# Kernel optimization log

Hardware: AMD Instinct MI355X
Metric: run time of the kernel (lower is better)

The kernel has to match this reference:

```python
import jax, jax.numpy as jnp
import numpy as np


def _build_cayley(metric):
    """Cayley table for the Clifford algebra with diagonal metric.
    Blades are indexed by bitmask (0=scalar, 1=e1, 2=e2, 3=e12, 4=e3, ...).
    cayley[i, j, k] = coefficient of blade j in the geometric product e_i * e_k.
    """
    n = len(metric)
    dim = 1 << n
    c = np.zeros((dim, dim, dim), dtype=np.float32)
    for a in range(dim):
        for b in range(dim):
            sign = 1.0
            tmp = a >> 1
            while tmp:  # count basis-vector swaps needed to sort e_a e_b
                if bin(tmp & b).count('1') & 1:
                    sign = -sign
                tmp >>= 1
            common = a & b
            for i in range(n):  # contract repeated basis vectors via the metric
                if common & (1 << i):
                    sign *= metric[i]
            c[a, a ^ b, b] = sign
    return c


def fast_einsum(q_einsum, cayley, k_einsum):
    # geometric product of two multivectors (same einsum as the torch.jit version)
    return jnp.einsum('...i,ijk,...k->...j', q_einsum, cayley, k_einsum)


def _embed_grade1(x, mv_dim):
    # embed a 3D vector as a grade-1 multivector: components at blade bitmasks 1, 2, 4
    mv = jnp.zeros(x.shape[:-1] + (mv_dim,), x.dtype)
    mv = mv.at[..., 1].set(x[..., 0])
    mv = mv.at[..., 2].set(x[..., 1])
    mv = mv.at[..., 4].set(x[..., 2])
    return mv


def setup_inputs() -> dict:
    key = jax.random.key(0)
    k1, k2 = jax.random.split(key)
    B, P, D = 4, 8192, 3
    return {
        'source_cloud': jax.random.normal(k1, (B, P, D), dtype=jnp.float32),
        'target_cloud': jax.random.normal(k2, (B, P, D), dtype=jnp.float32),
        'cayley': jnp.asarray(_build_cayley([1.0, 1.0, 1.0])),  # (8,8,8)
    }


def reference(source_cloud, target_cloud, cayley):
    # KNN (K=1) via full pairwise squared distances: (B, P1, P2)
    d2 = (jnp.sum(source_cloud * source_cloud, -1)[:, :, None]
          + jnp.sum(target_cloud * target_cloud, -1)[:, None, :]
          - 2.0 * jnp.einsum('bid,bjd->bij', source_cloud, target_cloud))
    idx = jnp.argmin(d2, axis=2)  # (B, P1) nearest-neighbor indices (non-differentiable)
    # knn_gather: nn[b, i] = target_cloud[b, idx[b, i]]
    nn = jnp.take_along_axis(target_cloud, idx[..., None], axis=1)  # (B, P1, 3)
    # multivector residual and geometric product with itself via the Cayley table
    diff_mv = _embed_grade1(source_cloud - nn, cayley.shape[0])  # (B, P1, 8)
    gp = fast_einsum(diff_mv, cayley, diff_mv)  # (B, P1, 8)
    # scalar part of v*v equals ||v||^2 under the Euclidean metric
    per_point = gp[..., 0]
    per_cloud = jnp.sum(per_point, axis=1)  # point_reduction='sum'
    return jnp.mean(per_cloud)  # batch_reduction='mean'
```

## Files before the change

### kernel.cpp

```cpp
#include <hip/hip_runtime.h>

#define BATCH 4
#define NPTS 8192
#define NTOT (BATCH * NPTS)

constexpr int THREADS   = 256;
constexpr int S_PER_THR = 8;
constexpr int SRC_CHUNK = THREADS * S_PER_THR;
constexpr int NSC       = NPTS / SRC_CHUNK;
constexpr int TGT_CHUNK = 256;
constexpr int NTC       = NPTS / TGT_CHUNK;
constexpr int R1_BLOCKS = 64;

__global__ __launch_bounds__(THREADS) void knn_partial_kernel(
        const float* __restrict__ src,
        const float* __restrict__ tgt,
        float* __restrict__ ws)
{
    int bid = blockIdx.x;
    int tc  = bid % NTC;
    int sc  = (bid / NTC) % NSC;
    int b   = bid / (NTC * NSC);

    __shared__ float4 tsh[TGT_CHUNK];

    {
        const float* tbase = tgt + ((size_t)b * NPTS + (size_t)tc * TGT_CHUNK) * 3;
        int k = threadIdx.x;
        float x = tbase[3 * k + 0];
        float y = tbase[3 * k + 1];
        float z = tbase[3 * k + 2];
        tsh[k] = make_float4(x, y, z, 0.5f * (x * x + y * y + z * z));
    }

    const float* sbase = src + ((size_t)b * NPTS + (size_t)sc * SRC_CHUNK) * 3;
    float sx[S_PER_THR], sy[S_PER_THR], sz[S_PER_THR], mb[S_PER_THR];
    #pragma unroll
    for (int s = 0; s < S_PER_THR; ++s) {
        int i = threadIdx.x + s * THREADS;
        sx[s] = sbase[3 * i + 0];
        sy[s] = sbase[3 * i + 1];
        sz[s] = sbase[3 * i + 2];
        mb[s] = INFINITY;
    }
    __syncthreads();

    #pragma unroll 4
    for (int j = 0; j < TGT_CHUNK; j += 2) {
        float4 t0 = tsh[j];
        float4 t1 = tsh[j + 1];
        #pragma unroll
        for (int s = 0; s < S_PER_THR; ++s) {
            float m0 = fmaf(-sx[s], t0.x, fmaf(-sy[s], t0.y, fmaf(-sz[s], t0.z, t0.w)));
            float m1 = fmaf(-sx[s], t1.x, fmaf(-sy[s], t1.y, fmaf(-sz[s], t1.z, t1.w)));
            mb[s] = fminf(mb[s], fminf(m0, m1));
        }
    }

    float* wbase = ws + (size_t)tc * NTOT + (size_t)b * NPTS + (size_t)sc * SRC_CHUNK;
    #pragma unroll
    for (int s = 0; s < S_PER_THR; ++s) {
        float hs = 0.5f * (sx[s] * sx[s] + sy[s] * sy[s] + sz[s] * sz[s]);
        wbase[threadIdx.x + s * THREADS] = mb[s] + hs;
    }
}

__global__ __launch_bounds__(256) void reduce1_kernel(
        const float* __restrict__ ws,
        float* __restrict__ partials)
{
    __shared__ float acc[256];
    int base = blockIdx.x * (NTOT / R1_BLOCKS);
    float a = 0.0f;
    #pragma unroll
    for (int p = 0; p < 2; ++p) {
        int i = base + threadIdx.x + p * 256;
        float m = INFINITY;
        #pragma unroll
        for (int sl = 0; sl < NTC; ++sl)
            m = fminf(m, ws[(size_t)sl * NTOT + i]);
        a += m;
    }
    acc[threadIdx.x] = a;
    __syncthreads();
    for (int off = 128; off > 0; off >>= 1) {
        if (threadIdx.x < off) acc[threadIdx.x] += acc[threadIdx.x + off];
        __syncthreads();
    }
    if (threadIdx.x == 0) partials[blockIdx.x] = acc[0];
}

__global__ __launch_bounds__(64) void reduce2_kernel(
        const float* __restrict__ partials,
        float* __restrict__ out)
{
    float v = partials[threadIdx.x];
    #pragma unroll
    for (int off = 32; off > 0; off >>= 1)
        v += __shfl_down(v, off, 64);
    if (threadIdx.x == 0) out[0] = v * 0.5f;
}

extern "C" void kernel_launch(void* const* d_in, const int* in_sizes, int n_in,
                              void* d_out, int out_size, void* d_ws, size_t ws_size,
                              hipStream_t stream) {
    const float* src = (const float*)d_in[0];
    const float* tgt = (const float*)d_in[1];
    float* out = (float*)d_out;
    float* ws  = (float*)d_ws;
    float* partials = (float*)((char*)d_ws + (size_t)NTC * NTOT * sizeof(float));

    knn_partial_kernel<<<BATCH * NSC * NTC, THREADS, 0, stream>>>(src, tgt, ws);
    reduce1_kernel<<<R1_BLOCKS, 256, 0, stream>>>(ws, partials);
    reduce2_kernel<<<1, 64, 0, stream>>>(partials, out);
}
```

Before: 33.17 us.

## Halve target chunk size and fuse final reductions with last-block atomic counter

Halves the target tile per block, which doubles the KNN grid to 512 blocks and adds occupancy launch bounds. This is meant to fill the GPU's compute units better, at the cost of twice as many partial-min slices to write and reduce. The two reduction kernels are merged into one: the last block to finish, found with an atomic counter and thread fences, does the final sum. That removes a launch but adds a memset to reset the counter. The reduction now uses 128 blocks, each handling one point per thread across 64 slices.

Result: slower. 49.25 us (+48.5%).

```diff
diff --git a/kernel.cpp b/kernel.cpp
--- a/kernel.cpp
+++ b/kernel.cpp
@@ -8,11 +8,11 @@
 constexpr int S_PER_THR = 8;
 constexpr int SRC_CHUNK = THREADS * S_PER_THR;
 constexpr int NSC       = NPTS / SRC_CHUNK;
-constexpr int TGT_CHUNK = 256;
+constexpr int TGT_CHUNK = 128;
 constexpr int NTC       = NPTS / TGT_CHUNK;
-constexpr int R1_BLOCKS = 64;
+constexpr int RBLOCKS   = 128;
 
-__global__ __launch_bounds__(THREADS) void knn_partial_kernel(
+__global__ __launch_bounds__(THREADS, 4) void knn_partial_kernel(
         const float* __restrict__ src,
         const float* __restrict__ tgt,
         float* __restrict__ ws)
@@ -24,7 +24,7 @@
 
     __shared__ float4 tsh[TGT_CHUNK];
 
-    {
+    if (threadIdx.x < TGT_CHUNK) {
         const float* tbase = tgt + ((size_t)b * NPTS + (size_t)tc * TGT_CHUNK) * 3;
         int k = threadIdx.x;
         float x = tbase[3 * k + 0];
@@ -65,40 +65,46 @@
     }
 }
 
-__global__ __launch_bounds__(256) void reduce1_kernel(
+__global__ __launch_bounds__(256) void reduce_kernel(
         const float* __restrict__ ws,
-        float* __restrict__ partials)
+        float* __restrict__ partials,
+        unsigned* __restrict__ counter,
+        float* __restrict__ out)
 {
     __shared__ float acc[256];
-    int base = blockIdx.x * (NTOT / R1_BLOCKS);
-    float a = 0.0f;
-    #pragma unroll
-    for (int p = 0; p < 2; ++p) {
-        int i = base + threadIdx.x + p * 256;
-        float m = INFINITY;
-        #pragma unroll
-        for (int sl = 0; sl < NTC; ++sl)
-            m = fminf(m, ws[(size_t)sl * NTOT + i]);
-        a += m;
-    }
-    acc[threadIdx.x] = a;
+    __shared__ unsigned my_rank;
+
+    int i = blockIdx.x * 256 + threadIdx.x;
+    float m = INFINITY;
+    #pragma unroll 8
+    for (int sl = 0; sl < NTC; ++sl)
+        m = fminf(m, ws[(size_t)sl * NTOT + i]);
+
+    acc[threadIdx.x] = m;
     __syncthreads();
     for (int off = 128; off > 0; off >>= 1) {
         if (threadIdx.x < off) acc[threadIdx.x] += acc[threadIdx.x + off];
         __syncthreads();
     }
-    if (threadIdx.x == 0) partials[blockIdx.x] = acc[0];
-}
+    if (threadIdx.x == 0) {
+        atomicExch(&partials[blockIdx.x], acc[0]);
+        __threadfence();
+        my_rank = atomicAdd(counter, 1u);
+    }
+    __syncthreads();
 
-__global__ __launch_bounds__(64) void reduce2_kernel(
-        const float* __restrict__ partials,
-        float* __restrict__ out)
-{
-    float v = partials[threadIdx.x];
-    #pragma unroll
-    for (int off = 32; off > 0; off >>= 1)
-        v += __shfl_down(v, off, 64);
-    if (threadIdx.x == 0) out[0] = v * 0.5f;
+    if (my_rank == RBLOCKS - 1) {
+        __threadfence();
+        float v = (threadIdx.x < RBLOCKS) ? atomicAdd(&partials[threadIdx.x], 0.0f)
+                                          : 0.0f;
+        acc[threadIdx.x] = v;
+        __syncthreads();
+        for (int off = 128; off > 0; off >>= 1) {
+            if (threadIdx.x < off) acc[threadIdx.x] += acc[threadIdx.x + off];
+            __syncthreads();
+        }
+        if (threadIdx.x == 0) out[0] = acc[0] * 0.5f;
+    }
 }
 
 extern "C" void kernel_launch(void* const* d_in, const int* in_sizes, int n_in,
@@ -107,10 +113,13 @@
     const float* src = (const float*)d_in[0];
     const float* tgt = (const float*)d_in[1];
     float* out = (float*)d_out;
-    float* ws  = (float*)d_ws;
-    float* partials = (float*)((char*)d_ws + (size_t)NTC * NTOT * sizeof(float));
+
+    float*    ws       = (float*)d_ws;
+    float*    partials = (float*)((char*)d_ws + (size_t)NTC * NTOT * 4);
+    unsigned* counter  = (unsigned*)((char*)partials + RBLOCKS * 4);
+
+    hipMemsetAsync(counter, 0, sizeof(unsigned), stream);
 
     knn_partial_kernel<<<BATCH * NSC * NTC, THREADS, 0, stream>>>(src, tgt, ws);
-    reduce1_kernel<<<R1_BLOCKS, 256, 0, stream>>>(ws, partials);
-    reduce2_kernel<<<1, 64, 0, stream>>>(partials, out);
+    reduce_kernel<<<RBLOCKS, 256, 0, stream>>>(ws, partials, counter, out);
 }
```

## Precompute packed target float4s in prep kernel and read them directly from global

Applied to the files above, without the earlier changes.

Adds a prep kernel that packs each target point into a float4 holding the coordinates and half its squared norm. The KNN kernel then drops its LDS staging and __syncthreads and reads those float4s straight from global memory as uniform loads. The target chunk is halved, which doubles the block count, and the reduction is reorganised into 128 blocks with one point per thread. The costs are an extra kernel launch, a larger workspace, twice as many partial-min slices to reduce, and global or scalar-cache loads in the inner loop instead of LDS reads.

Result: slower. 54.95 us (+65.7%).

```diff
diff --git a/kernel.cpp b/kernel.cpp
--- a/kernel.cpp
+++ b/kernel.cpp
@@ -8,30 +8,30 @@
 constexpr int S_PER_THR = 8;
 constexpr int SRC_CHUNK = THREADS * S_PER_THR;
 constexpr int NSC       = NPTS / SRC_CHUNK;
-constexpr int TGT_CHUNK = 256;
+constexpr int TGT_CHUNK = 128;
 constexpr int NTC       = NPTS / TGT_CHUNK;
-constexpr int R1_BLOCKS = 64;
+constexpr int RBLOCKS   = 128;
+
+__global__ __launch_bounds__(256) void prep_kernel(
+        const float* __restrict__ tgt, float4* __restrict__ tq) {
+    int i = blockIdx.x * 256 + threadIdx.x;
+    if (i < NTOT) {
+        float x = tgt[3 * i + 0];
+        float y = tgt[3 * i + 1];
+        float z = tgt[3 * i + 2];
+        tq[i] = make_float4(x, y, z, 0.5f * (x * x + y * y + z * z));
+    }
+}
 
 __global__ __launch_bounds__(THREADS) void knn_partial_kernel(
         const float* __restrict__ src,
-        const float* __restrict__ tgt,
+        const float4* __restrict__ tq,
         float* __restrict__ ws)
 {
     int bid = blockIdx.x;
     int tc  = bid % NTC;
     int sc  = (bid / NTC) % NSC;
     int b   = bid / (NTC * NSC);
-
-    __shared__ float4 tsh[TGT_CHUNK];
-
-    {
-        const float* tbase = tgt + ((size_t)b * NPTS + (size_t)tc * TGT_CHUNK) * 3;
-        int k = threadIdx.x;
-        float x = tbase[3 * k + 0];
-        float y = tbase[3 * k + 1];
-        float z = tbase[3 * k + 2];
-        tsh[k] = make_float4(x, y, z, 0.5f * (x * x + y * y + z * z));
-    }
 
     const float* sbase = src + ((size_t)b * NPTS + (size_t)sc * SRC_CHUNK) * 3;
     float sx[S_PER_THR], sy[S_PER_THR], sz[S_PER_THR], mb[S_PER_THR];
@@ -43,12 +43,13 @@
         sz[s] = sbase[3 * i + 2];
         mb[s] = INFINITY;
     }
-    __syncthreads();
+
+    const float4* tbase = tq + (size_t)b * NPTS + (size_t)tc * TGT_CHUNK;
 
     #pragma unroll 4
     for (int j = 0; j < TGT_CHUNK; j += 2) {
-        float4 t0 = tsh[j];
-        float4 t1 = tsh[j + 1];
+        float4 t0 = tbase[j];
+        float4 t1 = tbase[j + 1];
         #pragma unroll
         for (int s = 0; s < S_PER_THR; ++s) {
             float m0 = fmaf(-sx[s], t0.x, fmaf(-sy[s], t0.y, fmaf(-sz[s], t0.z, t0.w)));
@@ -70,18 +71,12 @@
         float* __restrict__ partials)
 {
     __shared__ float acc[256];
-    int base = blockIdx.x * (NTOT / R1_BLOCKS);
-    float a = 0.0f;
-    #pragma unroll
-    for (int p = 0; p < 2; ++p) {
-        int i = base + threadIdx.x + p * 256;
-        float m = INFINITY;
-        #pragma unroll
-        for (int sl = 0; sl < NTC; ++sl)
-            m = fminf(m, ws[(size_t)sl * NTOT + i]);
-        a += m;
-    }
-    acc[threadIdx.x] = a;
+    int i = blockIdx.x * 256 + threadIdx.x;
+    float m = INFINITY;
+    #pragma unroll 8
+    for (int sl = 0; sl < NTC; ++sl)
+        m = fminf(m, ws[(size_t)sl * NTOT + i]);
+    acc[threadIdx.x] = m;
     __syncthreads();
     for (int off = 128; off > 0; off >>= 1) {
         if (threadIdx.x < off) acc[threadIdx.x] += acc[threadIdx.x + off];
@@ -94,7 +89,7 @@
         const float* __restrict__ partials,
         float* __restrict__ out)
 {
-    float v = partials[threadIdx.x];
+    float v = partials[threadIdx.x] + partials[threadIdx.x + 64];
     #pragma unroll
     for (int off = 32; off > 0; off >>= 1)
         v += __shfl_down(v, off, 64);
@@ -107,10 +102,13 @@
     const float* src = (const float*)d_in[0];
     const float* tgt = (const float*)d_in[1];
     float* out = (float*)d_out;
-    float* ws  = (float*)d_ws;
-    float* partials = (float*)((char*)d_ws + (size_t)NTC * NTOT * sizeof(float));
 
-    knn_partial_kernel<<<BATCH * NSC * NTC, THREADS, 0, stream>>>(src, tgt, ws);
-    reduce1_kernel<<<R1_BLOCKS, 256, 0, stream>>>(ws, partials);
+    float4* tq       = (float4*)d_ws;
+    float*  ws       = (float*)((char*)d_ws + (size_t)NTOT * sizeof(float4));
+    float*  partials = (float*)((char*)ws + (size_t)NTC * NTOT * sizeof(float));
+
+    prep_kernel<<<NTOT / 256, 256, 0, stream>>>(tgt, tq);
+    knn_partial_kernel<<<BATCH * NSC * NTC, THREADS, 0, stream>>>(src, tq, ws);
+    reduce1_kernel<<<RBLOCKS, 256, 0, stream>>>(ws, partials);
     reduce2_kernel<<<1, 64, 0, stream>>>(partials, out);
 }
```

## Compute KNN distances with bf16 split-precision MFMA instead of scalar FMAs

Applied to the files above, without the earlier changes.

Moves the pairwise distance computation onto matrix cores. A prep kernel packs each target point as hi/lo bf16 pairs of its coordinates and half-norm, and the main kernel issues two 32x32x16 bf16 MFMAs per tile to emulate higher precision, then takes min over rows. The target set is split in two halves instead of 32 slabs, which shrinks the reduction work. This adds an extra kernel launch, wastes half of each wave's lanes (the upper 32 lanes feed zeros), and relies on hi/lo bf16 accuracy being enough for correct argmin distances.

After: 39.62 us. 1.19x slower.

```diff
diff --git a/kernel.cpp b/kernel.cpp
--- a/kernel.cpp
+++ b/kernel.cpp
@@ -4,82 +4,110 @@
 #define NPTS 8192
 #define NTOT (BATCH * NPTS)
 
-constexpr int THREADS   = 256;
-constexpr int S_PER_THR = 8;
-constexpr int SRC_CHUNK = THREADS * S_PER_THR;
-constexpr int NSC       = NPTS / SRC_CHUNK;
-constexpr int TGT_CHUNK = 256;
-constexpr int NTC       = NPTS / TGT_CHUNK;
-constexpr int R1_BLOCKS = 64;
+typedef __attribute__((ext_vector_type(8)))  short  short8;
+typedef __attribute__((ext_vector_type(16))) float  f32x16;
 
-__global__ __launch_bounds__(THREADS) void knn_partial_kernel(
-        const float* __restrict__ src,
-        const float* __restrict__ tgt,
-        float* __restrict__ ws)
+__device__ __forceinline__ unsigned short f2bf(float f) {
+    unsigned u = __float_as_uint(f);
+    unsigned r = u + 0x7FFFu + ((u >> 16) & 1u);
+    return (unsigned short)(r >> 16);
+}
+__device__ __forceinline__ float bf2f(unsigned short s) {
+    return __uint_as_float(((unsigned)s) << 16);
+}
+
+__global__ __launch_bounds__(256) void prep_kernel(
+        const float* __restrict__ tgt, short8* __restrict__ packed)
 {
-    int bid = blockIdx.x;
-    int tc  = bid % NTC;
-    int sc  = (bid / NTC) % NSC;
-    int b   = bid / (NTC * NSC);
+    int j = blockIdx.x * 256 + threadIdx.x;
+    float x = tgt[3*j+0], y = tgt[3*j+1], z = tgt[3*j+2];
+    float n = 0.5f * (x*x + y*y + z*z);
+    unsigned short hx = f2bf(x), hy = f2bf(y), hz = f2bf(z), hn = f2bf(n);
+    unsigned short lx = f2bf(x - bf2f(hx)), ly = f2bf(y - bf2f(hy)),
+                   lz = f2bf(z - bf2f(hz)), ln = f2bf(n - bf2f(hn));
+    short8 v = { (short)hx,(short)hy,(short)hz,(short)hn,
+                 (short)lx,(short)ly,(short)lz,(short)ln };
+    packed[j] = v;
+}
 
-    __shared__ float4 tsh[TGT_CHUNK];
+__global__ __launch_bounds__(256) void knn_mfma_kernel(
+        const float* __restrict__ src, const short8* __restrict__ packed,
+        float* __restrict__ slab)
+{
+    __shared__ short8 tlds[512];
 
-    {
-        const float* tbase = tgt + ((size_t)b * NPTS + (size_t)tc * TGT_CHUNK) * 3;
-        int k = threadIdx.x;
-        float x = tbase[3 * k + 0];
-        float y = tbase[3 * k + 1];
-        float z = tbase[3 * k + 2];
-        tsh[k] = make_float4(x, y, z, 0.5f * (x * x + y * y + z * z));
+    int gid   = blockIdx.x;
+    int half  = gid & 1;
+    int chunk = (gid >> 1) & 63;
+    int b     = gid >> 7;
+    int lane  = threadIdx.x & 63;
+    int wave  = threadIdx.x >> 6;
+    int col   = lane & 31;
+    bool lo   = (lane < 32);
+
+    int p_local = chunk * 128 + wave * 32 + col;
+
+    float sx = 0.f, sy = 0.f, sz = 0.f;
+    if (lo) {
+        const float* sp = src + ((size_t)b * NPTS + p_local) * 3;
+        sx = sp[0]; sy = sp[1]; sz = sp[2];
+    }
+    float ns2 = sx*sx + sy*sy + sz*sz;
+
+    float nx = -sx, ny = -sy, nz = -sz;
+    unsigned short hx = f2bf(nx), hy = f2bf(ny), hz = f2bf(nz);
+    unsigned short lx = f2bf(nx - bf2f(hx)), ly = f2bf(ny - bf2f(hy)),
+                   lz = f2bf(nz - bf2f(hz));
+    const short ONE = (short)0x3F80;
+    short8 B1 = {0,0,0,0,0,0,0,0}, B2 = {0,0,0,0,0,0,0,0};
+    if (lo) {
+        B1 = short8{ (short)hx,(short)hy,(short)hz, ONE,
+                     (short)hx,(short)hy,(short)hz, ONE };
+        B2 = short8{ (short)lx,(short)ly,(short)lz, 0,
+                     (short)lx,(short)ly,(short)lz, 0 };
     }
 
-    const float* sbase = src + ((size_t)b * NPTS + (size_t)sc * SRC_CHUNK) * 3;
-    float sx[S_PER_THR], sy[S_PER_THR], sz[S_PER_THR], mb[S_PER_THR];
+    const short8* tp = packed + (size_t)b * NPTS + (size_t)half * 4096;
+
+    float mb[8];
     #pragma unroll
-    for (int s = 0; s < S_PER_THR; ++s) {
-        int i = threadIdx.x + s * THREADS;
-        sx[s] = sbase[3 * i + 0];
-        sy[s] = sbase[3 * i + 1];
-        sz[s] = sbase[3 * i + 2];
-        mb[s] = INFINITY;
-    }
-    __syncthreads();
+    for (int i = 0; i < 8; ++i) mb[i] = INFINITY;
 
-    #pragma unroll 4
-    for (int j = 0; j < TGT_CHUNK; j += 2) {
-        float4 t0 = tsh[j];
-        float4 t1 = tsh[j + 1];
-        #pragma unroll
-        for (int s = 0; s < S_PER_THR; ++s) {
-            float m0 = fmaf(-sx[s], t0.x, fmaf(-sy[s], t0.y, fmaf(-sz[s], t0.z, t0.w)));
-            float m1 = fmaf(-sx[s], t1.x, fmaf(-sy[s], t1.y, fmaf(-sz[s], t1.z, t1.w)));
-            mb[s] = fminf(mb[s], fminf(m0, m1));
+    for (int g = 0; g < 8; ++g) {
+        __syncthreads();
+        tlds[threadIdx.x]       = tp[g*512 + threadIdx.x];
+        tlds[threadIdx.x + 256] = tp[g*512 + 256 + threadIdx.x];
+        __syncthreads();
+        #pragma unroll 4
+        for (int tt = 0; tt < 16; ++tt) {
+            short8 A = {0,0,0,0,0,0,0,0};
+            if (lo) A = tlds[tt*32 + col];
+            f32x16 c = {0,0,0,0,0,0,0,0,0,0,0,0,0,0,0,0};
+            c = __builtin_amdgcn_mfma_f32_32x32x16_bf16(A, B1, c, 0, 0, 0);
+            c = __builtin_amdgcn_mfma_f32_32x32x16_bf16(A, B2, c, 0, 0, 0);
+            #pragma unroll
+            for (int i = 0; i < 8; ++i)
+                mb[i] = fminf(mb[i], fminf(c[2*i], c[2*i+1]));
         }
     }
 
-    float* wbase = ws + (size_t)tc * NTOT + (size_t)b * NPTS + (size_t)sc * SRC_CHUNK;
-    #pragma unroll
-    for (int s = 0; s < S_PER_THR; ++s) {
-        float hs = 0.5f * (sx[s] * sx[s] + sy[s] * sy[s] + sz[s] * sz[s]);
-        wbase[threadIdx.x + s * THREADS] = mb[s] + hs;
-    }
+    float v = fminf(fminf(fminf(mb[0],mb[1]), fminf(mb[2],mb[3])),
+                    fminf(fminf(mb[4],mb[5]), fminf(mb[6],mb[7])));
+    v = fminf(v, __shfl_xor(v, 32, 64));
+    if (lo)
+        slab[(size_t)half * NTOT + (size_t)b * NPTS + p_local] = fmaf(2.0f, v, ns2);
 }
 
 __global__ __launch_bounds__(256) void reduce1_kernel(
-        const float* __restrict__ ws,
-        float* __restrict__ partials)
+        const float* __restrict__ slab, float* __restrict__ partials)
 {
     __shared__ float acc[256];
-    int base = blockIdx.x * (NTOT / R1_BLOCKS);
-    float a = 0.0f;
+    int base = blockIdx.x * 512;
+    float a = 0.f;
     #pragma unroll
     for (int p = 0; p < 2; ++p) {
         int i = base + threadIdx.x + p * 256;
-        float m = INFINITY;
-        #pragma unroll
-        for (int sl = 0; sl < NTC; ++sl)
-            m = fminf(m, ws[(size_t)sl * NTOT + i]);
-        a += m;
+        a += fminf(slab[i], slab[NTOT + i]);
     }
     acc[threadIdx.x] = a;
     __syncthreads();
@@ -91,14 +119,13 @@
 }
 
 __global__ __launch_bounds__(64) void reduce2_kernel(
-        const float* __restrict__ partials,
-        float* __restrict__ out)
+        const float* __restrict__ partials, float* __restrict__ out)
 {
     float v = partials[threadIdx.x];
     #pragma unroll
     for (int off = 32; off > 0; off >>= 1)
         v += __shfl_down(v, off, 64);
-    if (threadIdx.x == 0) out[0] = v * 0.5f;
+    if (threadIdx.x == 0) out[0] = v * 0.25f;
 }
 
 extern "C" void kernel_launch(void* const* d_in, const int* in_sizes, int n_in,
@@ -107,10 +134,13 @@
     const float* src = (const float*)d_in[0];
     const float* tgt = (const float*)d_in[1];
     float* out = (float*)d_out;
-    float* ws  = (float*)d_ws;
-    float* partials = (float*)((char*)d_ws + (size_t)NTC * NTOT * sizeof(float));
 
-    knn_partial_kernel<<<BATCH * NSC * NTC, THREADS, 0, stream>>>(src, tgt, ws);
-    reduce1_kernel<<<R1_BLOCKS, 256, 0, stream>>>(ws, partials);
+    short8* packed   = (short8*)d_ws;
+    float*  slab     = (float*)((char*)d_ws + (size_t)NTOT * sizeof(short8));
+    float*  partials = slab + 2 * NTOT;
+
+    prep_kernel<<<NTOT / 256, 256, 0, stream>>>(tgt, packed);
+    knn_mfma_kernel<<<512, 256, 0, stream>>>(src, packed, slab);
+    reduce1_kernel<<<64, 256, 0, stream>>>(slab, partials);
     reduce2_kernel<<<1, 64, 0, stream>>>(partials, out);
 }
```
